# Optimization experiments

Measured on AMD Instinct MI355X. Metric: run time of the kernel, lower is better.

Reference implementation:

```python
import jax, jax.numpy as jnp
import numpy as np

NUM_HEADS = 16
DIM_HEAD = 64
DIM = 1024
SCALE = DIM ** (-0.5)  # NOTE: source scales by model dim, not dim_head


def setup_inputs() -> dict:
    key = jax.random.key(0)
    ks = jax.random.split(key, 6)
    b, n, d = 2, 2048, DIM
    return {
        "x": jax.random.normal(ks[0], (b, n, d), dtype=jnp.float32),
        "mask": jnp.ones((b, n), dtype=bool),
        "Wq": jax.random.normal(ks[1], (NUM_HEADS * DIM_HEAD, d), dtype=jnp.float32) * 0.02,
        "Wk": jax.random.normal(ks[2], (DIM_HEAD, d), dtype=jnp.float32) * 0.02,
        "Wv": jax.random.normal(ks[3], (DIM_HEAD, d), dtype=jnp.float32) * 0.02,
        "Wfc": jax.random.normal(ks[4], (d, NUM_HEADS * DIM_HEAD), dtype=jnp.float32) * 0.02,
        "bfc": jnp.zeros((d,), dtype=jnp.float32),
    }


def reference(x, mask, Wq, Wk, Wv, Wfc, bfc):
    b, n, _ = x.shape
    # projections (nn.Linear: y = x @ W.T)
    q = (x @ Wq.T).reshape(b, n, NUM_HEADS, DIM_HEAD).transpose(0, 2, 1, 3)  # b h n d
    k = x @ Wk.T  # b n d  (single shared MQA head)
    v = x @ Wv.T  # b n d
    energy = jnp.einsum("bhid,bjd->bhij", q, k) * SCALE  # b h i j
    mask_value = -jnp.finfo(energy.dtype).max
    # input mask: k_mask is all ones in source, so only query rows are masked
    q_mask = mask[:, None, :, None]  # b 1 i 1
    energy = jnp.where(q_mask, energy, mask_value)
    # causal mask: positions j > i are masked (i == j since self-attention)
    i = jnp.arange(n)
    causal = i[:, None] < i[None, :]  # True where future
    energy = jnp.where(causal[None, None, :, :], mask_value, energy)
    attn = jax.nn.softmax(energy, axis=-1)
    # dropout_rate = 0.0 -> identity
    out = jnp.einsum("bhij,bjd->bhid", attn, v)
    out = out.transpose(0, 2, 1, 3).reshape(b, n, NUM_HEADS * DIM_HEAD)
    return out @ Wfc.T + bfc
```

## Files before the change

### kernel.cpp

```cpp
#include <hip/hip_runtime.h>
#include <math.h>

#define NH 16
#define DH 64
#define DM 1024
#define NS 2048
#define BB 2
#define MR (BB * NS)
#define LDQ 1152
#define C_EXP 0.0450842201f

typedef unsigned short u16;
typedef __attribute__((ext_vector_type(8))) short short8;
typedef __attribute__((ext_vector_type(4))) short short4v;
typedef __attribute__((ext_vector_type(4))) float floatx4;
typedef __attribute__((ext_vector_type(4))) u16 u16x4;

#if __has_builtin(__builtin_amdgcn_exp2f)
#define EXP2(x) __builtin_amdgcn_exp2f(x)
#else
#define EXP2(x) exp2f(x)
#endif

#define MFMA16(a, b, c) __builtin_amdgcn_mfma_f32_16x16x32_bf16((a), (b), (c), 0, 0, 0)

#if __has_builtin(__builtin_amdgcn_mfma_f32_16x16x16bf16_1k)
#define MFMAK16(a, b, c) __builtin_amdgcn_mfma_f32_16x16x16bf16_1k((a), (b), (c), 0, 0, 0)
#else
static __device__ __forceinline__ floatx4 mfmak16_(short4v a, short4v b, floatx4 c) {
  asm("v_mfma_f32_16x16x16_bf16 %0, %1, %2, %0" : "+v"(c) : "v"(a), "v"(b));
  return c;
}
#define MFMAK16(a, b, c) mfmak16_((a), (b), (c))
#endif

static __device__ __forceinline__ u16 f2bf(float f) {
  union { float f; unsigned u; } v; v.f = f;
  unsigned r = v.u + 0x7fffu + ((v.u >> 16) & 1u);
  return (u16)(r >> 16);
}
static __device__ __forceinline__ u16 f2bf_fast(float f) {
  union { float f; unsigned u; } v; v.f = f;
  return (u16)((v.u + 0x8000u) >> 16);
}

#define GLDS16(gp, lp)                                                        \
  __builtin_amdgcn_global_load_lds(                                           \
      (const __attribute__((address_space(1))) void*)(const void*)(gp),       \
      (__attribute__((address_space(3))) void*)(void*)(lp), 16, 0, 0)

__global__ __launch_bounds__(256) void cast_all(
    const float* __restrict__ x, const float* __restrict__ wq,
    const float* __restrict__ wk, const float* __restrict__ wv,
    const float* __restrict__ wfc, u16* __restrict__ xb,
    u16* __restrict__ wqkvb, u16* __restrict__ wfcb) {
  const int NX = MR * DM / 4, NQ = DM * DM / 4, NK = DH * DM / 4;
  int id = blockIdx.x * 256 + threadIdx.x;
  const float* src;
  u16* dst;
  int off;
  if (id < NX) { src = x; dst = xb; off = id; }
  else if (id < NX + NQ) { src = wq; dst = wqkvb; off = id - NX; }
  else if (id < NX + NQ + NK) { src = wk; dst = wqkvb + (size_t)DM * DM; off = id - NX - NQ; }
  else if (id < NX + NQ + 2 * NK) { src = wv; dst = wqkvb + (size_t)(DM + DH) * DM; off = id - NX - NQ - NK; }
  else { src = wfc; dst = wfcb; off = id - NX - NQ - 2 * NK; }
  float4 f = ((const float4*)src)[off];
  u16x4 o;
  o[0] = f2bf(f.x); o[1] = f2bf(f.y); o[2] = f2bf(f.z); o[3] = f2bf(f.w);
  ((u16x4*)dst)[off] = o;
}

__global__ __launch_bounds__(256) void gemm64(
    const u16* __restrict__ A, const u16* __restrict__ W,
    const float* __restrict__ bias, void* __restrict__ Cout,
    u16* __restrict__ vT, int M, int N, int K, int ldc, int out_bf16,
    int v_by) {
  __shared__ u16 As[2][64 * 32];
  __shared__ u16 Ws[2][64 * 32];
  const int tid = threadIdx.x;
  const int lane = tid & 63;
  const int lr = lane & 15, quad = lane >> 4;
  const int wave = tid >> 6, wr = wave >> 1, wc = wave & 1;

  const int lin = blockIdx.y * gridDim.x + blockIdx.x;
  const int xcd = lin & 7, slot = lin >> 3;
  const int bx = xcd * 8 + (slot & 7), by = slot >> 3;
  const int m0 = bx * 64, n0 = by * 64;

  const int srow = tid >> 2;
  const int scg = (tid & 3) ^ ((srow >> 1) & 3);
  const u16* gA = A + (size_t)(m0 + srow) * K + scg * 8;
  const u16* gW = W + (size_t)(n0 + srow) * K + scg * 8;
  const int lo = wave * 512;

  floatx4 acc[2][2] = {};
  const int nt = K >> 5;

  GLDS16(gA, &As[0][lo]);
  GLDS16(gW, &Ws[0][lo]);

  for (int t = 0; t < nt; ++t) {
    __syncthreads();
    if (t + 1 < nt) {
      const int ko = (t + 1) << 5;
      const int nb = (t + 1) & 1;
      GLDS16(gA + ko, &As[nb][lo]);
      GLDS16(gW + ko, &Ws[nb][lo]);
    }
    const u16* as = As[t & 1];
    const u16* ws = Ws[t & 1];
    short8 af[2], wf[2];
#pragma unroll
    for (int mi = 0; mi < 2; ++mi) {
      int rr = wr * 32 + mi * 16 + lr;
      af[mi] = *(const short8*)&as[rr * 32 + ((quad ^ ((rr >> 1) & 3)) << 3)];
    }
#pragma unroll
    for (int nj = 0; nj < 2; ++nj) {
      int rc = wc * 32 + nj * 16 + lr;
      wf[nj] = *(const short8*)&ws[rc * 32 + ((quad ^ ((rc >> 1) & 3)) << 3)];
    }
#pragma unroll
    for (int mi = 0; mi < 2; ++mi)
#pragma unroll
      for (int nj = 0; nj < 2; ++nj)
        acc[mi][nj] = MFMA16(af[mi], wf[nj], acc[mi][nj]);
  }

  if (v_by >= 0 && by == v_by) {
#pragma unroll
    for (int mi = 0; mi < 2; ++mi)
#pragma unroll
      for (int nj = 0; nj < 2; ++nj)
#pragma unroll
        for (int r = 0; r < 4; ++r)
          vT[(size_t)(wc * 32 + nj * 16 + lr) * MR + m0 + wr * 32 + mi * 16 +
             quad * 4 + r] = f2bf(acc[mi][nj][r]);
    return;
  }

#pragma unroll
  for (int mi = 0; mi < 2; ++mi) {
#pragma unroll
    for (int nj = 0; nj < 2; ++nj) {
      int col = n0 + wc * 32 + nj * 16 + lr;
      float badd = bias ? bias[col] : 0.f;
#pragma unroll
      for (int r = 0; r < 4; ++r) {
        int row = m0 + wr * 32 + mi * 16 + quad * 4 + r;
        float v = acc[mi][nj][r] + badd;
        if (out_bf16)
          ((u16*)Cout)[(size_t)row * ldc + col] = f2bf(v);
        else
          ((float*)Cout)[(size_t)row * ldc + col] = v;
      }
    }
  }
}

__global__ __launch_bounds__(256) void attn_mfma(
    const u16* __restrict__ qkv,
    const u16* __restrict__ vT,
    u16* __restrict__ aob) {
  __shared__ u16 Ks[2][128 * 64];
  __shared__ u16 Vt[2][64 * 128];

  const int b = blockIdx.z;
  const int p = blockIdx.x;
  const int tid = threadIdx.x;
  const int lane = tid & 63;
  const int lr = lane & 15, quad = lane >> 4;
  const int w = tid >> 6;
  const int head = blockIdx.y * 4 + w;
  const size_t rowb = (size_t)b * NS;
  const u16* kvK = qkv + rowb * LDQ + 1024;
  const u16* vTb = vT + rowb;

  int skrow[4], skcg[4], svrow[4], svcg[4], klo[4], vlo[4];
#pragma unroll
  for (int g = 0; g < 4; ++g) {
    const int ci = g * 256 + tid;
    skrow[g] = ci >> 3;
    skcg[g] = (ci & 7) ^ (skrow[g] & 7);
    svrow[g] = ci >> 4;
    svcg[g] = (ci & 15) ^ (svrow[g] & 15);
    klo[g] = (g * 256 + w * 64) * 8;
    vlo[g] = klo[g];
  }

  for (int phase = 0; phase < 2; ++phase) {
    const int s = (phase == 0) ? (63 - p) : p;
    const int i0q = s * 32;
    const int ntp = (s >> 2) + 1;
    const int irowA = i0q + lr;
    const int irowB = i0q + 16 + lr;

    const u16* qpA = qkv + (rowb + i0q + lr) * LDQ + head * DH;
    const u16* qpB = qpA + 16 * LDQ;
    short8 aqA0 = *(const short8*)(qpA + quad * 8);
    short8 aqA1 = *(const short8*)(qpA + 32 + quad * 8);
    short8 aqB0 = *(const short8*)(qpB + quad * 8);
    short8 aqB1 = *(const short8*)(qpB + 32 + quad * 8);

    floatx4 oA[4] = {}, oB[4] = {};
    float laccA = 0.f, laccB = 0.f;

#pragma unroll
    for (int g = 0; g < 4; ++g) {
      GLDS16(kvK + (size_t)skrow[g] * LDQ + skcg[g] * 8, &Ks[0][klo[g]]);
      GLDS16(vTb + (size_t)svrow[g] * MR + svcg[g] * 8, &Vt[0][vlo[g]]);
    }

    for (int t = 0; t < ntp; ++t) {
      const int buf = t & 1;
      __syncthreads();

      if (t + 1 < ntp) {
        const int j0n = (t + 1) * 128;
        const int nb2 = buf ^ 1;
#pragma unroll
        for (int g = 0; g < 4; ++g) {
          GLDS16(kvK + (size_t)(j0n + skrow[g]) * LDQ + skcg[g] * 8,
                 &Ks[nb2][klo[g]]);
          GLDS16(vTb + (size_t)svrow[g] * MR + j0n + svcg[g] * 8,
                 &Vt[nb2][vlo[g]]);
        }
      }

      const int j0 = t * 128;
      const u16* ksb = Ks[buf];
      const u16* vtb = Vt[buf];
      const bool lastt = (t == ntp - 1);

#pragma unroll
      for (int jb = 0; jb < 8; ++jb) {
        const int krow = jb * 16 + lr;
        short8 bk0 = *(const short8*)&ksb[krow * 64 + ((quad ^ (krow & 7)) << 3)];
        short8 bk1 = *(const short8*)&ksb[krow * 64 + (((4 + quad) ^ (krow & 7)) << 3)];
        floatx4 zA = {}, zB = {};
        zA = MFMA16(bk0, aqA0, zA);
        zA = MFMA16(bk1, aqA1, zA);
        zB = MFMA16(bk0, aqB0, zB);
        zB = MFMA16(bk1, aqB1, zB);

        const int kbase = j0 + jb * 16 + (quad << 2);
        short4v apA, apB;
#pragma unroll
        for (int r = 0; r < 4; ++r) {
          float peA = EXP2(zA[r] * C_EXP);
          float peB = EXP2(zB[r] * C_EXP);
          if (lastt && (kbase + r > irowA)) peA = 0.f;
          if (lastt && (kbase + r > irowB)) peB = 0.f;
          laccA += peA;
          laccB += peB;
          apA[r] = (short)f2bf_fast(peA);
          apB[r] = (short)f2bf_fast(peB);
        }

#pragma unroll
        for (int nb = 0; nb < 4; ++nb) {
          const int d = nb * 16 + lr;
          const int va = d * 128 + (((2 * jb + (quad >> 1)) ^ (d & 15)) << 3) +
                         ((quad & 1) << 2);
          short4v bv = *(const short4v*)&vtb[va];
          oA[nb] = MFMAK16(apA, bv, oA[nb]);
          oB[nb] = MFMAK16(apB, bv, oB[nb]);
        }
      }
    }

    laccA += __shfl_xor(laccA, 16);
    laccA += __shfl_xor(laccA, 32);
    laccB += __shfl_xor(laccB, 16);
    laccB += __shfl_xor(laccB, 32);
    float dA[4], dB[4];
#pragma unroll
    for (int r = 0; r < 4; ++r) {
      dA[r] = __shfl(laccA, (quad << 2) + r);
      dB[r] = __shfl(laccB, (quad << 2) + r);
    }

#pragma unroll
    for (int nb = 0; nb < 4; ++nb)
#pragma unroll
      for (int r = 0; r < 4; ++r) {
        const int col = head * DH + nb * 16 + lr;
        aob[(rowb + i0q + (quad << 2) + r) * DM + col] =
            f2bf(oA[nb][r] / dA[r]);
        aob[(rowb + i0q + 16 + (quad << 2) + r) * DM + col] =
            f2bf(oB[nb][r] / dB[r]);
      }

    __syncthreads();
  }
}

extern "C" void kernel_launch(void* const* d_in, const int* in_sizes, int n_in,
                              void* d_out, int out_size, void* d_ws, size_t ws_size,
                              hipStream_t stream) {
  const float* x = (const float*)d_in[0];
  const float* Wq = (const float*)d_in[2];
  const float* Wk = (const float*)d_in[3];
  const float* Wv = (const float*)d_in[4];
  const float* Wfc = (const float*)d_in[5];
  const float* bfc = (const float*)d_in[6];

  u16* xb = (u16*)d_ws;
  u16* wqkvb = xb + (size_t)MR * DM;
  u16* wfcb = wqkvb + (size_t)LDQ * DM;
  u16* qkv = wfcb + (size_t)DM * DM;
  u16* vT = qkv + (size_t)MR * LDQ;
  u16* aob = xb;

  cast_all<<<dim3((MR * DM + DM * DM * 2 + DH * DM * 2) / 1024), dim3(256), 0,
             stream>>>(x, Wq, Wk, Wv, Wfc, xb, wqkvb, wfcb);
  gemm64<<<dim3(MR / 64, LDQ / 64), dim3(256), 0, stream>>>(
      xb, wqkvb, nullptr, qkv, vT, MR, LDQ, DM, LDQ, 1, 17);
  attn_mfma<<<dim3(32, NH / 4, BB), dim3(256), 0, stream>>>(qkv, vT, aob);
  gemm64<<<dim3(MR / 64, DM / 64), dim3(256), 0, stream>>>(
      aob, wfcb, bfc, d_out, nullptr, MR, DM, DM, DM, 0, -1);
}
```

Measured before the change: 169.4 us.

## Split attention key tiles across two wave halves with LDS reduction

The attention kernel now runs 512 threads per block. Two groups of four waves each process half of every 128-key tile for the same heads, and their partial outputs and row sums are combined through shared memory before the final normalisation and store. This doubles the waves available to hide latency, and each thread issues fewer global-to-LDS loads. On the last causal tile the second half skips its work when all of its keys are masked. In exchange it adds an extra LDS reduction with barriers, a per-phase sync, and higher register pressure under the 512-thread launch bound.

```diff
diff --git a/kernel.cpp b/kernel.cpp
--- a/kernel.cpp
+++ b/kernel.cpp
@@ -158,12 +158,11 @@
   }
 }
 
-__global__ __launch_bounds__(256) void attn_mfma(
+__global__ __launch_bounds__(512) void attn_mfma(
     const u16* __restrict__ qkv,
     const u16* __restrict__ vT,
     u16* __restrict__ aob) {
-  __shared__ u16 Ks[2][128 * 64];
-  __shared__ u16 Vt[2][64 * 128];
+  __shared__ __align__(16) u16 smem[4 * 8192];
 
   const int b = blockIdx.z;
   const int p = blockIdx.x;
@@ -171,21 +170,23 @@
   const int lane = tid & 63;
   const int lr = lane & 15, quad = lane >> 4;
   const int w = tid >> 6;
-  const int head = blockIdx.y * 4 + w;
+  const int hl = w & 3;
+  const int half = w >> 2;
+  const int head = blockIdx.y * 4 + hl;
+  const int hb = half * 64;
   const size_t rowb = (size_t)b * NS;
   const u16* kvK = qkv + rowb * LDQ + 1024;
   const u16* vTb = vT + rowb;
 
-  int skrow[4], skcg[4], svrow[4], svcg[4], klo[4], vlo[4];
-#pragma unroll
-  for (int g = 0; g < 4; ++g) {
-    const int ci = g * 256 + tid;
+  int skrow[2], skcg[2], svrow[2], svcg[2], lo[2];
+#pragma unroll
+  for (int g = 0; g < 2; ++g) {
+    const int ci = g * 512 + tid;
     skrow[g] = ci >> 3;
     skcg[g] = (ci & 7) ^ (skrow[g] & 7);
     svrow[g] = ci >> 4;
     svcg[g] = (ci & 15) ^ (svrow[g] & 15);
-    klo[g] = (g * 256 + w * 64) * 8;
-    vlo[g] = klo[g];
+    lo[g] = (g * 512 + w * 64) * 8;
   }
 
   for (int phase = 0; phase < 2; ++phase) {
@@ -205,10 +206,11 @@
     floatx4 oA[4] = {}, oB[4] = {};
     float laccA = 0.f, laccB = 0.f;
 
-#pragma unroll
-    for (int g = 0; g < 4; ++g) {
-      GLDS16(kvK + (size_t)skrow[g] * LDQ + skcg[g] * 8, &Ks[0][klo[g]]);
-      GLDS16(vTb + (size_t)svrow[g] * MR + svcg[g] * 8, &Vt[0][vlo[g]]);
+    __syncthreads();
+#pragma unroll
+    for (int g = 0; g < 2; ++g) {
+      GLDS16(kvK + (size_t)skrow[g] * LDQ + skcg[g] * 8, &smem[lo[g]]);
+      GLDS16(vTb + (size_t)svrow[g] * MR + svcg[g] * 8, &smem[16384 + lo[g]]);
     }
 
     for (int t = 0; t < ntp; ++t) {
@@ -217,24 +219,26 @@
 
       if (t + 1 < ntp) {
         const int j0n = (t + 1) * 128;
-        const int nb2 = buf ^ 1;
-#pragma unroll
-        for (int g = 0; g < 4; ++g) {
+        const int nb2 = (buf ^ 1) * 8192;
+#pragma unroll
+        for (int g = 0; g < 2; ++g) {
           GLDS16(kvK + (size_t)(j0n + skrow[g]) * LDQ + skcg[g] * 8,
-                 &Ks[nb2][klo[g]]);
+                 &smem[nb2 + lo[g]]);
           GLDS16(vTb + (size_t)svrow[g] * MR + j0n + svcg[g] * 8,
-                 &Vt[nb2][vlo[g]]);
+                 &smem[16384 + nb2 + lo[g]]);
         }
       }
 
       const int j0 = t * 128;
-      const u16* ksb = Ks[buf];
-      const u16* vtb = Vt[buf];
+      const u16* ksb = smem + buf * 8192;
+      const u16* vtb = smem + 16384 + buf * 8192;
       const bool lastt = (t == ntp - 1);
 
-#pragma unroll
-      for (int jb = 0; jb < 8; ++jb) {
-        const int krow = jb * 16 + lr;
+      if (lastt && half == 1 && (s & 3) < 2) continue;
+
+#pragma unroll
+      for (int jb = 0; jb < 4; ++jb) {
+        const int krow = hb + jb * 16 + lr;
         short8 bk0 = *(const short8*)&ksb[krow * 64 + ((quad ^ (krow & 7)) << 3)];
         short8 bk1 = *(const short8*)&ksb[krow * 64 + (((4 + quad) ^ (krow & 7)) << 3)];
         floatx4 zA = {}, zB = {};
@@ -243,7 +247,7 @@
         zB = MFMA16(bk0, aqB0, zB);
         zB = MFMA16(bk1, aqB1, zB);
 
-        const int kbase = j0 + jb * 16 + (quad << 2);
+        const int kbase = j0 + hb + jb * 16 + (quad << 2);
         short4v apA, apB;
 #pragma unroll
         for (int r = 0; r < 4; ++r) {
@@ -260,7 +264,8 @@
 #pragma unroll
         for (int nb = 0; nb < 4; ++nb) {
           const int d = nb * 16 + lr;
-          const int va = d * 128 + (((2 * jb + (quad >> 1)) ^ (d & 15)) << 3) +
+          const int va = d * 128 +
+                         (((8 * half + 2 * jb + (quad >> 1)) ^ (d & 15)) << 3) +
                          ((quad & 1) << 2);
           short4v bv = *(const short4v*)&vtb[va];
           oA[nb] = MFMAK16(apA, bv, oA[nb]);
@@ -273,25 +278,50 @@
     laccA += __shfl_xor(laccA, 32);
     laccB += __shfl_xor(laccB, 16);
     laccB += __shfl_xor(laccB, 32);
-    float dA[4], dB[4];
-#pragma unroll
-    for (int r = 0; r < 4; ++r) {
-      dA[r] = __shfl(laccA, (quad << 2) + r);
-      dB[r] = __shfl(laccB, (quad << 2) + r);
-    }
-
-#pragma unroll
-    for (int nb = 0; nb < 4; ++nb)
+
+    __syncthreads();
+    float* M = (float*)smem;
+    float* Mh = M + hl * 34 * 64;
+    if (half == 1) {
+#pragma unroll
+      for (int nb = 0; nb < 4; ++nb)
+#pragma unroll
+        for (int r = 0; r < 4; ++r) {
+          Mh[(nb * 4 + r) * 64 + lane] = oA[nb][r];
+          Mh[(16 + nb * 4 + r) * 64 + lane] = oB[nb][r];
+        }
+      Mh[32 * 64 + lane] = laccA;
+      Mh[33 * 64 + lane] = laccB;
+    }
+    __syncthreads();
+    if (half == 0) {
+#pragma unroll
+      for (int nb = 0; nb < 4; ++nb)
+#pragma unroll
+        for (int r = 0; r < 4; ++r) {
+          oA[nb][r] += Mh[(nb * 4 + r) * 64 + lane];
+          oB[nb][r] += Mh[(16 + nb * 4 + r) * 64 + lane];
+        }
+      laccA += Mh[32 * 64 + lane];
+      laccB += Mh[33 * 64 + lane];
+
+      float dA[4], dB[4];
 #pragma unroll
       for (int r = 0; r < 4; ++r) {
-        const int col = head * DH + nb * 16 + lr;
-        aob[(rowb + i0q + (quad << 2) + r) * DM + col] =
-            f2bf(oA[nb][r] / dA[r]);
-        aob[(rowb + i0q + 16 + (quad << 2) + r) * DM + col] =
-            f2bf(oB[nb][r] / dB[r]);
+        dA[r] = __shfl(laccA, (quad << 2) + r);
+        dB[r] = __shfl(laccB, (quad << 2) + r);
       }
-
-    __syncthreads();
+#pragma unroll
+      for (int nb = 0; nb < 4; ++nb)
+#pragma unroll
+        for (int r = 0; r < 4; ++r) {
+          const int col = head * DH + nb * 16 + lr;
+          aob[(rowb + i0q + (quad << 2) + r) * DM + col] =
+              f2bf(oA[nb][r] / dA[r]);
+          aob[(rowb + i0q + 16 + (quad << 2) + r) * DM + col] =
+              f2bf(oB[nb][r] / dB[r]);
+        }
+    }
   }
 }
 
@@ -316,7 +346,7 @@
              stream>>>(x, Wq, Wk, Wv, Wfc, xb, wqkvb, wfcb);
   gemm64<<<dim3(MR / 64, LDQ / 64), dim3(256), 0, stream>>>(
       xb, wqkvb, nullptr, qkv, vT, MR, LDQ, DM, LDQ, 1, 17);
-  attn_mfma<<<dim3(32, NH / 4, BB), dim3(256), 0, stream>>>(qkv, vT, aob);
+  attn_mfma<<<dim3(32, NH / 4, BB), dim3(512), 0, stream>>>(qkv, vT, aob);
   gemm64<<<dim3(MR / 64, DM / 64), dim3(256), 0, stream>>>(
       aob, wfcb, bfc, d_out, nullptr, MR, DM, DM, DM, 0, -1);
 }
```

Measured after the change: 152.9 us, median of 4. 9.7% less time.
